# Kernel tuning notes

Hardware: AMD Instinct MI355X
Metric: run time of the kernel (lower is better)

## Reference

```python
import jax, jax.numpy as jnp
import numpy as np

BATCH, NVIS, NHID, NCOND = 4096, 1024, 4096, 512


def setup_inputs() -> dict:
    key = jax.random.key(0)
    ks = jax.random.split(key, 6)
    return {
        "visible_data": jax.random.uniform(ks[0], (BATCH, NVIS), dtype=jnp.float32),
        "cond_data": jax.random.normal(ks[1], (BATCH, NCOND), dtype=jnp.float32),
        # uniform noise replaces torch.bernoulli's internal RNG: sample = (noise < p)
        "noise": jax.random.uniform(ks[2], (BATCH, NHID), dtype=jnp.float32),
        "W": jax.random.normal(ks[3], (NVIS, NHID), dtype=jnp.float32) * 0.1,
        "b": jnp.zeros((1, NVIS), dtype=jnp.float32),
        "c": jnp.zeros((1, NHID), dtype=jnp.float32),
        "A": jax.random.normal(ks[4], (NCOND, NVIS), dtype=jnp.float32) * 0.1,
        "B": jax.random.normal(ks[5], (NCOND, NHID), dtype=jnp.float32) * 0.1,
    }


def reference(visible_data, cond_data, noise, W, b, c, A, B):
    # sample_h_given_vu: sigmoid(v@W + u@B + c), bernoulli sample via uniform noise
    h1_mean = jax.nn.sigmoid(visible_data @ W + cond_data @ B + c)  # [B, nhid]
    h1_sample = (noise < h1_mean).astype(h1_mean.dtype)
    # sample_v_given_hu (binary): L1-normalized exp == softmax, then argmax one-hot
    pre = h1_sample @ W.T + cond_data @ A + b  # [B, nvis]
    v1_mean = jax.nn.softmax(pre, axis=1)
    max_idx = jnp.argmax(v1_mean, axis=1)
    v1_sample = jax.nn.one_hot(max_idx, pre.shape[1], dtype=pre.dtype)
    return v1_sample
```

## Files before the change

### kernel.cpp

```cpp
#include <hip/hip_runtime.h>
#include <math.h>

static constexpr int BATCH = 4096;
static constexpr int NVIS  = 1024;
static constexpr int NHID  = 4096;
static constexpr int NCOND = 512;

typedef __attribute__((ext_vector_type(8))) short bf16x8;
typedef __attribute__((ext_vector_type(4))) float f32x4;
typedef __attribute__((ext_vector_type(4))) int   i32x4;

static constexpr unsigned HCAP = 131072;
static constexpr unsigned RCAP = 256;
static constexpr size_t MB = 1u << 20;

static constexpr size_t F_WT0   = 0;
static constexpr size_t F_WT1   = F_WT0  + 8*MB;
static constexpr size_t F_BMT0  = F_WT1  + 8*MB;
static constexpr size_t F_BMT1  = F_BMT0 + 4*MB;
static constexpr size_t F_AT0   = F_BMT1 + 4*MB;
static constexpr size_t F_AT1   = F_AT0  + 1*MB;
static constexpr size_t F_V0    = F_AT1  + 1*MB;
static constexpr size_t F_V1    = F_V0   + 8*MB;
static constexpr size_t F_U0    = F_V1   + 8*MB;
static constexpr size_t F_U1    = F_U0   + 4*MB;
static constexpr size_t F_QH    = F_U1   + 4*MB;
static constexpr size_t F_QL    = F_QH   + 4*MB;
static constexpr size_t F_SINV  = F_QL   + 4*MB;
static constexpr size_t F_H     = F_SINV + 8*MB;
static constexpr size_t F_BB    = F_H    + 32*MB;
static constexpr size_t F_HFLAG = F_BB   + 1*MB;
static constexpr size_t F_RFLAG = F_HFLAG + 512*1024;
static constexpr size_t F_RBEST = F_RFLAG + 16384;
static constexpr size_t F_CNT   = F_RBEST + 16384;
static constexpr size_t F_PREB  = F_CNT  + 256;
static constexpr size_t WS_FULL = F_PREB + 2*MB;

__device__ __forceinline__ void gload16(const void* g, void* l) {
    __builtin_amdgcn_global_load_lds(
        (const __attribute__((address_space(1))) void*)g,
        (__attribute__((address_space(3))) void*)l, 16, 0, 0);
}

__device__ __forceinline__ void split1(float x, unsigned short& hi, unsigned short& lo) {
    unsigned u = __float_as_uint(x);
    unsigned r = u + 0x7FFFu + ((u >> 16) & 1u);
    hi = (unsigned short)(r >> 16);
    float rem = x - __uint_as_float(r & 0xFFFF0000u);
    unsigned u2 = __float_as_uint(rem);
    unsigned r2 = u2 + 0x7FFFu + ((u2 >> 16) & 1u);
    lo = (unsigned short)(r2 >> 16);
}

__device__ __forceinline__ void merge3(float& b, unsigned& ix, float& s,
                                       float b2, unsigned i2, float s2) {
    if (b2 > b || (b2 == b && i2 < ix)) { s = fmaxf(b, s2); b = b2; ix = i2; }
    else                                { s = fmaxf(s, b2); }
}

#define SFENCE() __builtin_amdgcn_sched_barrier(0)
#define BARRIER() do { asm volatile("" ::: "memory"); SFENCE(); \
                       __builtin_amdgcn_s_barrier(); SFENCE(); \
                       asm volatile("" ::: "memory"); } while (0)
#define VMW(N) asm volatile("s_waitcnt vmcnt(" #N ")" ::: "memory")
#define LGKM0() do { asm volatile("s_waitcnt lgkmcnt(0)" ::: "memory"); SFENCE(); } while (0)

__global__ void kz_zero(unsigned* c) { if (threadIdx.x < 64) c[threadIdx.x] = 0; }

__global__ __launch_bounds__(256) void transpose_split(
    const float* __restrict__ src, int R, int C,
    unsigned short* __restrict__ d0, unsigned short* __restrict__ d1) {
    __shared__ float tile[32][33];
    const int c0 = blockIdx.x * 32, r0 = blockIdx.y * 32;
    const int tx = threadIdx.x & 31, ty = threadIdx.x >> 5;
#pragma unroll
    for (int e = 0; e < 4; ++e)
        tile[ty + e * 8][tx] = src[(size_t)(r0 + ty + e * 8) * C + c0 + tx];
    __syncthreads();
#pragma unroll
    for (int e = 0; e < 4; ++e) {
        int c = c0 + ty + e * 8;
        unsigned short hi, lo;
        split1(tile[tx][ty + e * 8], hi, lo);
        d0[(size_t)c * R + r0 + tx] = hi;
        d1[(size_t)c * R + r0 + tx] = lo;
    }
}

__global__ __launch_bounds__(256) void transpose_f32(
    const float* __restrict__ src, int R, int C, float* __restrict__ dst) {
    __shared__ float tile[32][33];
    const int c0 = blockIdx.x * 32, r0 = blockIdx.y * 32;
    const int tx = threadIdx.x & 31, ty = threadIdx.x >> 5;
#pragma unroll
    for (int e = 0; e < 4; ++e)
        tile[ty + e * 8][tx] = src[(size_t)(r0 + ty + e * 8) * C + c0 + tx];
    __syncthreads();
#pragma unroll
    for (int e = 0; e < 4; ++e)
        dst[(size_t)(c0 + ty + e * 8) * R + r0 + tx] = tile[tx][ty + e * 8];
}

__global__ __launch_bounds__(256) void split_planes(
    const float* __restrict__ src, int n4,
    unsigned short* __restrict__ p0, unsigned short* __restrict__ p1) {
    for (int i = blockIdx.x * 256 + threadIdx.x; i < n4; i += gridDim.x * 256) {
        float4 v = ((const float4*)src)[i];
        unsigned short h0,h1,h2,h3,l0,l1,l2,l3;
        split1(v.x,h0,l0); split1(v.y,h1,l1); split1(v.z,h2,l2); split1(v.w,h3,l3);
        ((ushort4*)p0)[i] = make_ushort4(h0,h1,h2,h3);
        ((ushort4*)p1)[i] = make_ushort4(l0,l1,l2,l3);
    }
}

__global__ __launch_bounds__(256) void quantize_w(
    const float* __restrict__ W, signed char* __restrict__ QH,
    signed char* __restrict__ QL, float* __restrict__ SINV) {
    __shared__ float red[256];
    const int i = blockIdx.x, t = threadIdx.x;
    const float* row = W + (size_t)i * NHID;
    float4 v[4];
    float mx = 0.f;
#pragma unroll
    for (int e = 0; e < 4; ++e) {
        v[e] = *(const float4*)(row + e * 1024 + t * 4);
        mx = fmaxf(mx, fmaxf(fmaxf(fabsf(v[e].x), fabsf(v[e].y)),
                             fmaxf(fabsf(v[e].z), fabsf(v[e].w))));
    }
    red[t] = mx; __syncthreads();
    for (int s = 128; s; s >>= 1) {
        if (t < s) red[t] = fmaxf(red[t], red[t + s]);
        __syncthreads();
    }
    const float rm = fmaxf(red[0], 1e-30f);
    const float sc = 32256.f / rm;
    if (t == 0) SINV[i] = rm / 32256.f;
#pragma unroll
    for (int e = 0; e < 4; ++e) {
        const float* pv = (const float*)&v[e];
        unsigned ph = 0, pl = 0;
#pragma unroll
        for (int j = 0; j < 4; ++j) {
            int wq = (int)lrintf(pv[j] * sc);
            int hi = (wq + 128) >> 8;
            int lo = wq - (hi << 8);
            ph |= ((unsigned)hi & 0xFFu) << (8 * j);
            pl |= ((unsigned)lo & 0xFFu) << (8 * j);
        }
        *(unsigned*)(QH + (size_t)i * NHID + e * 1024 + t * 4) = ph;
        *(unsigned*)(QL + (size_t)i * NHID + e * 1024 + t * 4) = pl;
    }
}

__global__ __launch_bounds__(512, 1) void k1_4p(
    const float* __restrict__ noise,
    const unsigned short* __restrict__ V0, const unsigned short* __restrict__ V1,
    const unsigned short* __restrict__ U0, const unsigned short* __restrict__ U1,
    const unsigned short* __restrict__ WT0, const unsigned short* __restrict__ WT1,
    const unsigned short* __restrict__ BmT0, const unsigned short* __restrict__ BmT1,
    const float* __restrict__ cvec, unsigned char* __restrict__ hout,
    unsigned* __restrict__ hcnt, unsigned* __restrict__ hflag)
{
    __shared__ __align__(16) unsigned short As0[2][256][32], As1[2][256][32],
                                            Bs0[2][256][32], Bs1[2][256][32];
    const int t = threadIdx.x, lane = t & 63, wid = t >> 6;
    const int g = lane >> 4, cc = lane & 15;
    const int wrow = wid >> 2, wcol = wid & 3;
    const int pc = (g ^ ((cc >> 1) & 3)) * 8;
    const int nwg = gridDim.x * gridDim.y;
    const int bid = blockIdx.y * gridDim.x + blockIdx.x;
    const int q = nwg >> 3;
    const int swz = (bid & 7) * q + (bid >> 3);
    const int b0 = (swz / gridDim.x) * 256;
    const int j0 = (swz % gridDim.x) * 256;

    auto srcs = [&](int ks, const unsigned short*& A0_, const unsigned short*& A1_,
                    const unsigned short*& B0_, const unsigned short*& B1_,
                    int& K_, int& k0_) {
        if (ks < 32) { A0_ = V0; A1_ = V1; B0_ = WT0; B1_ = WT1; K_ = 1024; k0_ = ks * 32; }
        else         { A0_ = U0; A1_ = U1; B0_ = BmT0; B1_ = BmT1; K_ = 512; k0_ = (ks - 32) * 32; }
    };
    auto stageA = [&](int ks, int bi, int mh) {
        const unsigned short *A0_, *A1_, *B0_, *B1_; int K_, k0_;
        srcs(ks, A0_, A1_, B0_, B1_, K_, k0_);
        int rl = t >> 2, s = t & 3;
        int r = mh * 128 + rl;
        int sc = s ^ ((r >> 1) & 3);
        size_t ga = (size_t)(b0 + r) * K_ + k0_ + sc * 8;
        size_t ldd = (size_t)mh * 4096 + (size_t)t * 8;
        gload16(A0_ + ga, &As0[bi][0][0] + ldd);
        gload16(A1_ + ga, &As1[bi][0][0] + ldd);
    };
    auto stageB = [&](int ks, int bi, int nh) {
        const unsigned short *A0_, *A1_, *B0_, *B1_; int K_, k0_;
        srcs(ks, A0_, A1_, B0_, B1_, K_, k0_);
        int rl = t >> 2, s = t & 3;
        int r = nh * 128 + rl;
        int sc = s ^ ((r >> 1) & 3);
        size_t gb = (size_t)(j0 + r) * K_ + k0_ + sc * 8;
        size_t ldd = (size_t)nh * 4096 + (size_t)t * 8;
        gload16(B0_ + gb, &Bs0[bi][0][0] + ldd);
        gload16(B1_ + gb, &Bs1[bi][0][0] + ldd);
    };

    f32x4 acc[8][4] = {};
    bf16x8 a0q[4], a1q[4];
    bf16x8 b0a[2][2], b1a[2][2];

    auto readA = [&](int cur, int mh) {
#pragma unroll
        for (int k = 0; k < 4; ++k) {
            int r = wrow * 128 + (4 * mh + k) * 16 + cc;
            a0q[k] = *(const bf16x8*)&As0[cur][r][pc];
            a1q[k] = *(const bf16x8*)&As1[cur][r][pc];
        }
    };
    auto readB = [&](int cur, int nh) {
#pragma unroll
        for (int k = 0; k < 2; ++k) {
            int n = wcol * 64 + (2 * nh + k) * 16 + cc;
            b0a[nh][k] = *(const bf16x8*)&Bs0[cur][n][pc];
            b1a[nh][k] = *(const bf16x8*)&Bs1[cur][n][pc];
        }
    };
    auto mfma24 = [&](int mh, int nh) {
#pragma unroll
        for (int k = 0; k < 4; ++k)
#pragma unroll
            for (int n = 0; n < 2; ++n) {
                f32x4 c = acc[4 * mh + k][2 * nh + n];
                c = __builtin_amdgcn_mfma_f32_16x16x32_bf16(a0q[k], b0a[nh][n], c, 0, 0, 0);
                c = __builtin_amdgcn_mfma_f32_16x16x32_bf16(a0q[k], b1a[nh][n], c, 0, 0, 0);
                c = __builtin_amdgcn_mfma_f32_16x16x32_bf16(a1q[k], b0a[nh][n], c, 0, 0, 0);
                acc[4 * mh + k][2 * nh + n] = c;
            }
    };

    stageA(0, 0, 0); stageB(0, 0, 0); stageB(0, 0, 1); stageA(0, 0, 1);
    VMW(4);
    BARRIER();

    for (int tt = 0; tt < 48; ++tt) {
        const int cur = tt & 1, nb = cur ^ 1;
        const bool pre = (tt + 1 < 48);
        readA(cur, 0); readB(cur, 0);
        if (pre) stageA(tt + 1, nb, 0);
        BARRIER();
        LGKM0();
        __builtin_amdgcn_s_setprio(1); mfma24(0, 0); __builtin_amdgcn_s_setprio(0);
        if (pre) { VMW(4); } else { VMW(2); }
        BARRIER();
        readB(cur, 1);
        if (pre) stageB(tt + 1, nb, 0);
        BARRIER();
        LGKM0();
        __builtin_amdgcn_s_setprio(1); mfma24(0, 1); __builtin_amdgcn_s_setprio(0);
        if (pre) { VMW(4); } else { VMW(0); }
        BARRIER();
        readA(cur, 1);
        if (pre) stageB(tt + 1, nb, 1);
        BARRIER();
        LGKM0();
        __builtin_amdgcn_s_setprio(1); mfma24(1, 0); __builtin_amdgcn_s_setprio(0);
        BARRIER();
        if (pre) stageA(tt + 1, nb, 1);
        BARRIER();
        LGKM0();
        __builtin_amdgcn_s_setprio(1); mfma24(1, 1); __builtin_amdgcn_s_setprio(0);
        if (pre) { VMW(4); }
        BARRIER();
    }

#pragma unroll
    for (int ni = 0; ni < 4; ++ni) {
        int j = j0 + wcol * 64 + ni * 16 + cc;
        float cj = cvec[j];
#pragma unroll
        for (int mi = 0; mi < 8; ++mi) {
#pragma unroll
            for (int i = 0; i < 4; ++i) {
                int b = b0 + wrow * 128 + mi * 16 + g * 4 + i;
                float z = acc[mi][ni][i] + cj;
                float m = 1.0f / (1.0f + __expf(-z));
                float nv = noise[(size_t)b * NHID + j];
                hout[(size_t)b * NHID + j] = (nv < m) ? (unsigned char)1 : (unsigned char)0;
                if (fabsf(nv - m) < 2.5e-4f) {
                    unsigned p = atomicAdd(hcnt, 1u);
                    if (p < HCAP) hflag[p] = ((unsigned)b << 12) | (unsigned)j;
                }
            }
        }
    }
}

__global__ __launch_bounds__(512, 2) void k2_i8(
    const unsigned char* __restrict__ hbf,
    const unsigned short* __restrict__ U0, const unsigned short* __restrict__ U1,
    const signed char* __restrict__ QH, const signed char* __restrict__ QL,
    const float* __restrict__ SINV,
    const unsigned short* __restrict__ AT0, const unsigned short* __restrict__ AT1,
    const float* __restrict__ bvec, float4* __restrict__ blockbest)
{
    __shared__ __align__(16) char smem[32768];
    __shared__ float4 mbuf[4][128];
    const int t = threadIdx.x, lane = t & 63, wid = t >> 6;
    const int g = lane >> 4, cc = lane & 15;
    const int wrow = wid >> 2, wcol = wid & 3;
    const int pcb = (g ^ ((cc >> 1) & 3)) * 16;
    const int nwg = gridDim.x * gridDim.y;
    const int bid = blockIdx.y * gridDim.x + blockIdx.x;
    const int q = nwg >> 3;
    const int swz = (bid & 7) * q + (bid >> 3);
    const int b0 = (swz / gridDim.x) * 128;
    const int i0 = (swz % gridDim.x) * 128;

    char* Ah  = smem;
    char* Qhs = smem + 8192;
    char* Qls = smem + 16384;

    i32x4 ah[4][2] = {}, al[4][2] = {};

    for (int k0 = 0; k0 < NHID; k0 += 64) {
        __syncthreads();
        {
            int r = t >> 2, s = t & 3, sc = s ^ ((r >> 1) & 3);
            size_t off = (size_t)r * 64 + s * 16;
            gload16(hbf + (size_t)(b0 + r) * NHID + k0 + sc * 16, Ah + off);
            gload16(QH + (size_t)(i0 + r) * NHID + k0 + sc * 16, Qhs + off);
            gload16(QL + (size_t)(i0 + r) * NHID + k0 + sc * 16, Qls + off);
        }
        __syncthreads();
        i32x4 bh[2], bl[2];
#pragma unroll
        for (int ni = 0; ni < 2; ++ni) {
            int n = wcol * 32 + ni * 16 + cc;
            bh[ni] = *(const i32x4*)(Qhs + (size_t)n * 64 + pcb);
            bl[ni] = *(const i32x4*)(Qls + (size_t)n * 64 + pcb);
        }
#pragma unroll
        for (int mi = 0; mi < 4; ++mi) {
            i32x4 a = *(const i32x4*)(Ah + (size_t)(wrow * 64 + mi * 16 + cc) * 64 + pcb);
#pragma unroll
            for (int ni = 0; ni < 2; ++ni) {
                ah[mi][ni] = __builtin_amdgcn_mfma_i32_16x16x64_i8(a, bh[ni], ah[mi][ni], 0, 0, 0);
                al[mi][ni] = __builtin_amdgcn_mfma_i32_16x16x64_i8(a, bl[ni], al[mi][ni], 0, 0, 0);
            }
        }
    }
    f32x4 acc[4][2];
#pragma unroll
    for (int ni = 0; ni < 2; ++ni) {
        int col = i0 + wcol * 32 + ni * 16 + cc;
        float sv = SINV[col];
#pragma unroll
        for (int mi = 0; mi < 4; ++mi)
#pragma unroll
            for (int e = 0; e < 4; ++e)
                acc[mi][ni][e] = fmaf(256.f, (float)ah[mi][ni][e], (float)al[mi][ni][e]) * sv;
    }

    char* As0 = smem;
    char* As1 = smem + 8192;
    char* Bs0 = smem + 16384;
    char* Bs1 = smem + 24576;
    for (int k0 = 0; k0 < NCOND; k0 += 32) {
        __syncthreads();
        {
            int r = t >> 2, s = t & 3, sc = s ^ ((r >> 1) & 3);
            size_t off = (size_t)r * 64 + s * 16;
            size_t ga = (size_t)(b0 + r) * NCOND + k0 + sc * 8;
            gload16(U0 + ga, As0 + off);
            gload16(U1 + ga, As1 + off);
            size_t go = (size_t)(i0 + r) * NCOND + k0 + sc * 8;
            gload16(AT0 + go, Bs0 + off);
            gload16(AT1 + go, Bs1 + off);
        }
        __syncthreads();
        bf16x8 bb0[2], bb1[2];
#pragma unroll
        for (int ni = 0; ni < 2; ++ni) {
            int n = wcol * 32 + ni * 16 + cc;
            bb0[ni] = *(const bf16x8*)(Bs0 + (size_t)n * 64 + pcb);
            bb1[ni] = *(const bf16x8*)(Bs1 + (size_t)n * 64 + pcb);
        }
#pragma unroll
        for (int mi = 0; mi < 4; ++mi) {
            int r = wrow * 64 + mi * 16 + cc;
            bf16x8 a0 = *(const bf16x8*)(As0 + (size_t)r * 64 + pcb);
            bf16x8 a1 = *(const bf16x8*)(As1 + (size_t)r * 64 + pcb);
#pragma unroll
            for (int ni = 0; ni < 2; ++ni) {
                acc[mi][ni] = __builtin_amdgcn_mfma_f32_16x16x32_bf16(a0, bb0[ni], acc[mi][ni], 0, 0, 0);
                acc[mi][ni] = __builtin_amdgcn_mfma_f32_16x16x32_bf16(a0, bb1[ni], acc[mi][ni], 0, 0, 0);
                acc[mi][ni] = __builtin_amdgcn_mfma_f32_16x16x32_bf16(a1, bb0[ni], acc[mi][ni], 0, 0, 0);
            }
        }
    }

#pragma unroll
    for (int ni = 0; ni < 2; ++ni) {
        int colb = i0 + wcol * 32 + ni * 16 + cc;
        float bb = bvec[colb];
#pragma unroll
        for (int mi = 0; mi < 4; ++mi)
#pragma unroll
            for (int i = 0; i < 4; ++i) acc[mi][ni][i] += bb;
    }
#pragma unroll
    for (int mi = 0; mi < 4; ++mi) {
#pragma unroll
        for (int i = 0; i < 4; ++i) {
            float best = acc[mi][0][i];
            unsigned bidx = (unsigned)(i0 + wcol * 32 + cc);
            float sec = -3.4e38f;
            merge3(best, bidx, sec, acc[mi][1][i],
                   (unsigned)(i0 + wcol * 32 + 16 + cc), -3.4e38f);
#pragma unroll
            for (int m = 1; m < 16; m <<= 1) {
                float ob = __shfl_xor(best, m);
                unsigned oi = __shfl_xor(bidx, m);
                float os = __shfl_xor(sec, m);
                merge3(best, bidx, sec, ob, oi, os);
            }
            if (cc == 0)
                mbuf[wcol][wrow * 64 + mi * 16 + g * 4 + i] =
                    make_float4(best, sec, __uint_as_float(bidx), 0.f);
        }
    }
    __syncthreads();
    if (t < 128) {
        float4 f0 = mbuf[0][t];
        float best = f0.x, sec = f0.y;
        unsigned bidx = __float_as_uint(f0.z);
#pragma unroll
        for (int wq = 1; wq < 4; ++wq) {
            float4 fq = mbuf[wq][t];
            merge3(best, bidx, sec, fq.x, __float_as_uint(fq.z), fq.y);
        }
        blockbest[(size_t)(b0 + t) * 8 + (unsigned)(i0 >> 7)] =
            make_float4(best, sec, __uint_as_float(bidx), 0.f);
    }
}

__global__ __launch_bounds__(256) void k5_recheck_h(
    const float* __restrict__ vd, const float* __restrict__ cd, const float* __restrict__ noise,
    const float* __restrict__ WTf, const float* __restrict__ BmTf, const float* __restrict__ cvec,
    const unsigned* __restrict__ hcnt, const unsigned* __restrict__ hflag,
    unsigned char* __restrict__ h) {
    const int gw = (blockIdx.x * 256 + threadIdx.x) >> 6, lane = threadIdx.x & 63;
    const int nw = gridDim.x * 4;
    unsigned n = *hcnt; if (n > HCAP) n = HCAP;
    for (unsigned e = gw; e < n; e += nw) {
        unsigned p = hflag[e];
        int b = p >> 12, j = p & 4095;
        double s = 0.0;
        for (int k = lane; k < NVIS; k += 64)
            s += (double)vd[(size_t)b * NVIS + k] * (double)WTf[(size_t)j * NVIS + k];
        for (int k = lane; k < NCOND; k += 64)
            s += (double)cd[(size_t)b * NCOND + k] * (double)BmTf[(size_t)j * NCOND + k];
        for (int m = 32; m; m >>= 1) s += __shfl_xor(s, m);
        if (lane == 0) {
            double z = s + (double)cvec[j];
            double mm = 1.0 / (1.0 + exp(-z));
            h[(size_t)b * NHID + j] =
                ((double)noise[(size_t)b * NHID + j] < mm) ? (unsigned char)1 : (unsigned char)0;
        }
    }
}

__global__ __launch_bounds__(256) void k3_merge8(
    const float4* __restrict__ blockbest, unsigned* __restrict__ rowbest,
    unsigned* __restrict__ rcnt, unsigned* __restrict__ rowflag) {
    const int t = threadIdx.x;
    const int row = blockIdx.x * 32 + (t >> 3), e = t & 7;
    float4 f = blockbest[(size_t)row * 8 + e];
    float best = f.x, sec = f.y;
    unsigned idx = __float_as_uint(f.z);
#pragma unroll
    for (int m = 1; m < 8; m <<= 1) {
        float ob = __shfl_xor(best, m);
        unsigned oi = __shfl_xor(idx, m);
        float os = __shfl_xor(sec, m);
        merge3(best, idx, sec, ob, oi, os);
    }
    if (e == 0) {
        rowbest[row] = idx;
        if (best - sec < 4e-3f) {
            unsigned p = atomicAdd(rcnt, 1u);
            if (p < 4096) rowflag[p] = (unsigned)row;
        }
    }
}

__global__ __launch_bounds__(256) void k_onehot(const unsigned* __restrict__ rowbest,
                                                float* __restrict__ out) {
    const int row = blockIdx.x;
    const unsigned idx = rowbest[row];
    const int base = threadIdx.x * 4;
    float4 o;
    o.x = (base + 0 == (int)idx) ? 1.f : 0.f;
    o.y = (base + 1 == (int)idx) ? 1.f : 0.f;
    o.z = (base + 2 == (int)idx) ? 1.f : 0.f;
    o.w = (base + 3 == (int)idx) ? 1.f : 0.f;
    *(float4*)(out + (size_t)row * NVIS + base) = o;
}

__global__ __launch_bounds__(256) void k6_rows_pre(
    const unsigned char* __restrict__ h, const float* __restrict__ cd,
    const float* __restrict__ W, const float* __restrict__ ATf, const float* __restrict__ bvec,
    const unsigned* __restrict__ rcnt, const unsigned* __restrict__ rowflag,
    double* __restrict__ prebuf) {
    const int gw = (blockIdx.x * 256 + threadIdx.x) >> 6, lane = threadIdx.x & 63;
    const int nw = gridDim.x * 4;
    unsigned n = *rcnt; if (n > RCAP) n = RCAP;
    for (unsigned e = gw; e < n * 1024u; e += nw) {
        int ri = e >> 10, i = e & 1023;
        int b = (int)rowflag[ri];
        double s = 0.0;
        for (int k = lane; k < NHID; k += 64) {
            double hv = h[(size_t)b * NHID + k] ? 1.0 : 0.0;
            s += hv * (double)W[(size_t)i * NHID + k];
        }
        for (int k = lane; k < NCOND; k += 64)
            s += (double)cd[(size_t)b * NCOND + k] * (double)ATf[(size_t)i * NCOND + k];
        for (int m = 32; m; m >>= 1) s += __shfl_xor(s, m);
        if (lane == 0) prebuf[(size_t)ri * 1024 + i] = s + (double)bvec[i];
    }
}

__global__ __launch_bounds__(256) void k6_rows_argmax(
    const unsigned* __restrict__ rcnt, const unsigned* __restrict__ rowflag,
    const double* __restrict__ prebuf, float* __restrict__ out) {
    __shared__ double sv[256];
    __shared__ int si[256];
    unsigned n = *rcnt; if (n > RCAP) n = RCAP;
    const int t = threadIdx.x;
    for (unsigned ri = blockIdx.x; ri < n; ri += gridDim.x) {
        const int row = (int)rowflag[ri];
        const double* pr = prebuf + (size_t)ri * 1024;
        double best = pr[t * 4];
        int bi = t * 4;
#pragma unroll
        for (int e = 1; e < 4; ++e) {
            double v = pr[t * 4 + e];
            if (v > best) { best = v; bi = t * 4 + e; }
        }
        sv[t] = best; si[t] = bi;
        __syncthreads();
        for (int s = 128; s; s >>= 1) {
            if (t < s) {
                double v2 = sv[t + s]; int i2 = si[t + s];
                if (v2 > sv[t] || (v2 == sv[t] && i2 < si[t])) { sv[t] = v2; si[t] = i2; }
            }
            __syncthreads();
        }
        const int amax = si[0];
        const int base = t * 4;
        float4 o;
        o.x = (base + 0 == amax) ? 1.f : 0.f;
        o.y = (base + 1 == amax) ? 1.f : 0.f;
        o.z = (base + 2 == amax) ? 1.f : 0.f;
        o.w = (base + 3 == amax) ? 1.f : 0.f;
        *(float4*)(out + (size_t)row * NVIS + base) = o;
        __syncthreads();
    }
}

extern "C" void kernel_launch(void* const* d_in, const int* in_sizes, int n_in,
                              void* d_out, int out_size, void* d_ws, size_t ws_size,
                              hipStream_t stream) {
    const float* vd = (const float*)d_in[0];
    const float* cd = (const float*)d_in[1];
    const float* nz = (const float*)d_in[2];
    const float* W  = (const float*)d_in[3];
    const float* bv = (const float*)d_in[4];
    const float* cv = (const float*)d_in[5];
    const float* Am = (const float*)d_in[6];
    const float* Bm = (const float*)d_in[7];
    float* out = (float*)d_out;
    char* w = (char*)d_ws;

    unsigned short* WT0  = (unsigned short*)(w + F_WT0);
    unsigned short* WT1  = (unsigned short*)(w + F_WT1);
    unsigned short* BmT0 = (unsigned short*)(w + F_BMT0);
    unsigned short* BmT1 = (unsigned short*)(w + F_BMT1);
    unsigned short* AT0  = (unsigned short*)(w + F_AT0);
    unsigned short* AT1  = (unsigned short*)(w + F_AT1);
    unsigned short* V0   = (unsigned short*)(w + F_V0);
    unsigned short* V1   = (unsigned short*)(w + F_V1);
    unsigned short* U0   = (unsigned short*)(w + F_U0);
    unsigned short* U1   = (unsigned short*)(w + F_U1);
    signed char*    QH   = (signed char*)(w + F_QH);
    signed char*    QL   = (signed char*)(w + F_QL);
    float*          SINV = (float*)(w + F_SINV);
    unsigned char*  hbf  = (unsigned char*)(w + F_H);
    float4*   blockbest  = (float4*)(w + F_BB);
    unsigned* hflag      = (unsigned*)(w + F_HFLAG);
    unsigned* rowflag    = (unsigned*)(w + F_RFLAG);
    unsigned* rowbest    = (unsigned*)(w + F_RBEST);
    unsigned* counters   = (unsigned*)(w + F_CNT);
    double*   prebuf     = (double*)(w + F_PREB);
    unsigned* hcnt = &counters[0];
    unsigned* rcnt = &counters[1];
    float* WTf32  = (float*)(w + F_V0);
    float* BmTf32 = (float*)(w + F_WT0);
    float* ATf32  = (float*)(w + F_WT1);

    dim3 blk(256);
    kz_zero<<<1, 64, 0, stream>>>(counters);
    transpose_split<<<dim3(NHID / 32, NVIS / 32), blk, 0, stream>>>(W, NVIS, NHID, WT0, WT1);
    transpose_split<<<dim3(NHID / 32, NCOND / 32), blk, 0, stream>>>(Bm, NCOND, NHID, BmT0, BmT1);
    transpose_split<<<dim3(NVIS / 32, NCOND / 32), blk, 0, stream>>>(Am, NCOND, NVIS, AT0, AT1);
    split_planes<<<2048, blk, 0, stream>>>(vd, BATCH * NVIS / 4, V0, V1);
    split_planes<<<2048, blk, 0, stream>>>(cd, BATCH * NCOND / 4, U0, U1);
    quantize_w<<<NVIS, blk, 0, stream>>>(W, QH, QL, SINV);
    k1_4p<<<dim3(NHID / 256, BATCH / 256), 512, 0, stream>>>(
        nz, V0, V1, U0, U1, WT0, WT1, BmT0, BmT1, cv, hbf, hcnt, hflag);
    transpose_f32<<<dim3(NHID / 32, NVIS / 32), blk, 0, stream>>>(W, NVIS, NHID, WTf32);
    transpose_f32<<<dim3(NHID / 32, NCOND / 32), blk, 0, stream>>>(Bm, NCOND, NHID, BmTf32);
    transpose_f32<<<dim3(NVIS / 32, NCOND / 32), blk, 0, stream>>>(Am, NCOND, NVIS, ATf32);
    k5_recheck_h<<<256, blk, 0, stream>>>(vd, cd, nz, WTf32, BmTf32, cv, hcnt, hflag, hbf);
    k2_i8<<<dim3(NVIS / 128, BATCH / 128), 512, 0, stream>>>(
        hbf, U0, U1, QH, QL, SINV, AT0, AT1, bv, blockbest);
    k3_merge8<<<BATCH / 32, blk, 0, stream>>>(blockbest, rowbest, rcnt, rowflag);
    k_onehot<<<BATCH, blk, 0, stream>>>(rowbest, out);
    k6_rows_pre<<<512, blk, 0, stream>>>(hbf, cd, W, ATf32, bv, rcnt, rowflag, prebuf);
    k6_rows_argmax<<<64, blk, 0, stream>>>(rcnt, rowflag, prebuf, out);
}
```

Baseline: 512.9 us.

## Replace double-buffered K=32 pipeline with single-buffered K=64 tiles in first GEMM

The first GEMM kernel drops its hand-scheduled double-buffered pipeline, with its many barriers and explicit waitcnts, in favour of a single LDS buffer holding K=64 per stage. That halves the number of outer iterations. It also uses a new 8-way XOR swizzle across 128-byte rows. The aim is fewer barriers and larger, more efficient loads per stage. The cost is that global loads no longer overlap with MFMA compute, since each tile is loaded and then consumed between two __syncthreads.

Result: no change. 505.0 us (-1.6%).

```diff
diff --git a/kernel.cpp b/kernel.cpp
--- a/kernel.cpp
+++ b/kernel.cpp
@@ -58,13 +58,6 @@
     else                                { s = fmaxf(s, b2); }
 }
 
-#define SFENCE() __builtin_amdgcn_sched_barrier(0)
-#define BARRIER() do { asm volatile("" ::: "memory"); SFENCE(); \
-                       __builtin_amdgcn_s_barrier(); SFENCE(); \
-                       asm volatile("" ::: "memory"); } while (0)
-#define VMW(N) asm volatile("s_waitcnt vmcnt(" #N ")" ::: "memory")
-#define LGKM0() do { asm volatile("s_waitcnt lgkmcnt(0)" ::: "memory"); SFENCE(); } while (0)
-
 __global__ void kz_zero(unsigned* c) { if (threadIdx.x < 64) c[threadIdx.x] = 0; }
 
 __global__ __launch_bounds__(256) void transpose_split(
@@ -152,7 +145,7 @@
     }
 }
 
-__global__ __launch_bounds__(512, 1) void k1_4p(
+__global__ __launch_bounds__(512, 1) void k1_b64(
     const float* __restrict__ noise,
     const unsigned short* __restrict__ V0, const unsigned short* __restrict__ V1,
     const unsigned short* __restrict__ U0, const unsigned short* __restrict__ U1,
@@ -161,12 +154,11 @@
     const float* __restrict__ cvec, unsigned char* __restrict__ hout,
     unsigned* __restrict__ hcnt, unsigned* __restrict__ hflag)
 {
-    __shared__ __align__(16) unsigned short As0[2][256][32], As1[2][256][32],
-                                            Bs0[2][256][32], Bs1[2][256][32];
+    __shared__ __align__(16) unsigned short As0[256][64], As1[256][64],
+                                            Bs0[256][64], Bs1[256][64];
     const int t = threadIdx.x, lane = t & 63, wid = t >> 6;
     const int g = lane >> 4, cc = lane & 15;
     const int wrow = wid >> 2, wcol = wid & 3;
-    const int pc = (g ^ ((cc >> 1) & 3)) * 8;
     const int nwg = gridDim.x * gridDim.y;
     const int bid = blockIdx.y * gridDim.x + blockIdx.x;
     const int q = nwg >> 3;
@@ -174,53 +166,27 @@
     const int b0 = (swz / gridDim.x) * 256;
     const int j0 = (swz % gridDim.x) * 256;
 
-    auto srcs = [&](int ks, const unsigned short*& A0_, const unsigned short*& A1_,
-                    const unsigned short*& B0_, const unsigned short*& B1_,
-                    int& K_, int& k0_) {
-        if (ks < 32) { A0_ = V0; A1_ = V1; B0_ = WT0; B1_ = WT1; K_ = 1024; k0_ = ks * 32; }
-        else         { A0_ = U0; A1_ = U1; B0_ = BmT0; B1_ = BmT1; K_ = 512; k0_ = (ks - 32) * 32; }
-    };
-    auto stageA = [&](int ks, int bi, int mh) {
-        const unsigned short *A0_, *A1_, *B0_, *B1_; int K_, k0_;
-        srcs(ks, A0_, A1_, B0_, B1_, K_, k0_);
-        int rl = t >> 2, s = t & 3;
-        int r = mh * 128 + rl;
-        int sc = s ^ ((r >> 1) & 3);
-        size_t ga = (size_t)(b0 + r) * K_ + k0_ + sc * 8;
-        size_t ldd = (size_t)mh * 4096 + (size_t)t * 8;
-        gload16(A0_ + ga, &As0[bi][0][0] + ldd);
-        gload16(A1_ + ga, &As1[bi][0][0] + ldd);
-    };
-    auto stageB = [&](int ks, int bi, int nh) {
-        const unsigned short *A0_, *A1_, *B0_, *B1_; int K_, k0_;
-        srcs(ks, A0_, A1_, B0_, B1_, K_, k0_);
-        int rl = t >> 2, s = t & 3;
-        int r = nh * 128 + rl;
-        int sc = s ^ ((r >> 1) & 3);
-        size_t gb = (size_t)(j0 + r) * K_ + k0_ + sc * 8;
-        size_t ldd = (size_t)nh * 4096 + (size_t)t * 8;
-        gload16(B0_ + gb, &Bs0[bi][0][0] + ldd);
-        gload16(B1_ + gb, &Bs1[bi][0][0] + ldd);
-    };
-
     f32x4 acc[8][4] = {};
     bf16x8 a0q[4], a1q[4];
     bf16x8 b0a[2][2], b1a[2][2];
 
-    auto readA = [&](int cur, int mh) {
+    auto lba = [&](int r, int kk) {
+        return (size_t)r * 128 + (size_t)(((kk << 2) | g) ^ (r & 7)) * 16;
+    };
+    auto readA = [&](int mh, int kk) {
 #pragma unroll
         for (int k = 0; k < 4; ++k) {
             int r = wrow * 128 + (4 * mh + k) * 16 + cc;
-            a0q[k] = *(const bf16x8*)&As0[cur][r][pc];
-            a1q[k] = *(const bf16x8*)&As1[cur][r][pc];
+            a0q[k] = *(const bf16x8*)((const char*)As0 + lba(r, kk));
+            a1q[k] = *(const bf16x8*)((const char*)As1 + lba(r, kk));
         }
     };
-    auto readB = [&](int cur, int nh) {
+    auto readB = [&](int nh, int kk) {
 #pragma unroll
         for (int k = 0; k < 2; ++k) {
             int n = wcol * 64 + (2 * nh + k) * 16 + cc;
-            b0a[nh][k] = *(const bf16x8*)&Bs0[cur][n][pc];
-            b1a[nh][k] = *(const bf16x8*)&Bs1[cur][n][pc];
+            b0a[nh][k] = *(const bf16x8*)((const char*)Bs0 + lba(n, kk));
+            b1a[nh][k] = *(const bf16x8*)((const char*)Bs1 + lba(n, kk));
         }
     };
     auto mfma24 = [&](int mh, int nh) {
@@ -236,39 +202,34 @@
             }
     };
 
-    stageA(0, 0, 0); stageB(0, 0, 0); stageB(0, 0, 1); stageA(0, 0, 1);
-    VMW(4);
-    BARRIER();
-
-    for (int tt = 0; tt < 48; ++tt) {
-        const int cur = tt & 1, nb = cur ^ 1;
-        const bool pre = (tt + 1 < 48);
-        readA(cur, 0); readB(cur, 0);
-        if (pre) stageA(tt + 1, nb, 0);
-        BARRIER();
-        LGKM0();
-        __builtin_amdgcn_s_setprio(1); mfma24(0, 0); __builtin_amdgcn_s_setprio(0);
-        if (pre) { VMW(4); } else { VMW(2); }
-        BARRIER();
-        readB(cur, 1);
-        if (pre) stageB(tt + 1, nb, 0);
-        BARRIER();
-        LGKM0();
-        __builtin_amdgcn_s_setprio(1); mfma24(0, 1); __builtin_amdgcn_s_setprio(0);
-        if (pre) { VMW(4); } else { VMW(0); }
-        BARRIER();
-        readA(cur, 1);
-        if (pre) stageB(tt + 1, nb, 1);
-        BARRIER();
-        LGKM0();
-        __builtin_amdgcn_s_setprio(1); mfma24(1, 0); __builtin_amdgcn_s_setprio(0);
-        BARRIER();
-        if (pre) stageA(tt + 1, nb, 1);
-        BARRIER();
-        LGKM0();
-        __builtin_amdgcn_s_setprio(1); mfma24(1, 1); __builtin_amdgcn_s_setprio(0);
-        if (pre) { VMW(4); }
-        BARRIER();
+    for (int tt = 0; tt < 24; ++tt) {
+        const unsigned short *A0_, *A1_, *B0_, *B1_; int K_, k0_;
+        if (tt < 16) { A0_ = V0; A1_ = V1; B0_ = WT0; B1_ = WT1; K_ = 1024; k0_ = tt * 64; }
+        else         { A0_ = U0; A1_ = U1; B0_ = BmT0; B1_ = BmT1; K_ = 512; k0_ = (tt - 16) * 64; }
+        __syncthreads();
+#pragma unroll
+        for (int e = 0; e < 4; ++e) {
+            int idx = t + e * 512;
+            int r = idx >> 3, p = idx & 7;
+            int s = p ^ (r & 7);
+            size_t ga = (size_t)(b0 + r) * K_ + k0_ + s * 8;
+            size_t gb = (size_t)(j0 + r) * K_ + k0_ + s * 8;
+            size_t ldd = (size_t)idx * 16;
+            gload16(A0_ + ga, (char*)As0 + ldd);
+            gload16(A1_ + ga, (char*)As1 + ldd);
+            gload16(B0_ + gb, (char*)Bs0 + ldd);
+            gload16(B1_ + gb, (char*)Bs1 + ldd);
+        }
+        __syncthreads();
+#pragma unroll
+        for (int kk = 0; kk < 2; ++kk) {
+            readA(0, kk); readB(0, kk);
+            __builtin_amdgcn_s_setprio(1); mfma24(0, 0); __builtin_amdgcn_s_setprio(0);
+            readB(1, kk);
+            __builtin_amdgcn_s_setprio(1); mfma24(0, 1); __builtin_amdgcn_s_setprio(0);
+            readA(1, kk);
+            __builtin_amdgcn_s_setprio(1); mfma24(1, 0); mfma24(1, 1); __builtin_amdgcn_s_setprio(0);
+        }
     }
 
 #pragma unroll
@@ -614,7 +575,7 @@
     split_planes<<<2048, blk, 0, stream>>>(vd, BATCH * NVIS / 4, V0, V1);
     split_planes<<<2048, blk, 0, stream>>>(cd, BATCH * NCOND / 4, U0, U1);
     quantize_w<<<NVIS, blk, 0, stream>>>(W, QH, QL, SINV);
-    k1_4p<<<dim3(NHID / 256, BATCH / 256), 512, 0, stream>>>(
+    k1_b64<<<dim3(NHID / 256, BATCH / 256), 512, 0, stream>>>(
         nz, V0, V1, U0, U1, WT0, WT1, BmT0, BmT1, cv, hbf, hcnt, hflag);
     transpose_f32<<<dim3(NHID / 32, NVIS / 32), blk, 0, stream>>>(W, NVIS, NHID, WTf32);
     transpose_f32<<<dim3(NHID / 32, NCOND / 32), blk, 0, stream>>>(Bm, NCOND, NHID, BmTf32);
```
